# Kernel tuning notes

Hardware: AMD Instinct MI355X
Metric: run time of the kernel (lower is better)

## Reference

```python
import jax, jax.numpy as jnp
import numpy as np

B, S, D, H = 4, 4096, 1024, 16
DV = D // H


def setup_inputs() -> dict:
    key = jax.random.key(0)
    ks = jax.random.split(key, 8)
    def gl(k, shape):  # glorot-uniform-ish init
        fan_in, fan_out = shape[0], shape[-1]
        lim = np.sqrt(6.0 / (fan_in + fan_out)).astype(np.float32)
        return jax.random.uniform(k, shape, jnp.float32, -lim, lim)
    return {
        "q": jax.random.normal(ks[0], (B, S, D), jnp.float32),
        "k": jax.random.normal(ks[1], (B, S, D), jnp.float32),
        "v": jax.random.normal(ks[2], (B, S, D), jnp.float32),
        "wq": gl(ks[3], (D, H)), "bq": jnp.zeros((H,), jnp.float32),
        "wk": gl(ks[4], (D, H)), "bk": jnp.zeros((H,), jnp.float32),
        "wv": gl(ks[5], (D, D)), "bv": jnp.zeros((D,), jnp.float32),
        "wo": gl(ks[6], (D, D)), "bo": jnp.zeros((D,), jnp.float32),
    }


def reference(q, k, v, wq, bq, wk, bk, wv, bv, wo, bo):
    b, s, d = q.shape
    h = wq.shape[1]
    dv = d // h
    # per-head scalar queries/keys, sigmoid feature map phi
    qh = jax.nn.sigmoid(q @ wq + bq)                 # (B,S,H)
    kh = jax.nn.sigmoid(k @ wk + bk)                 # (B,S,H)
    vh = (v @ wv + bv).reshape(b, s, h, dv)          # (B,S,H,DV)
    # phi(k)^T @ v contracts seq -> per-head summary (B,H,DV)
    kv = jnp.einsum("bsh,bshd->bhd", kh, vh)
    # NOTE: original tf code cumsums over axis=1 of (B,H,1,DV): the HEAD axis
    state = jnp.cumsum(kv, axis=1)                   # (B,H,DV)
    # phi(q) @ state, broadcast over seq
    out_h = jnp.einsum("bsh,bhd->bshd", qh, state)   # (B,S,H,DV)
    concat = out_h.reshape(b, s, d)
    return concat @ wo + bo                          # (B,S,D)
```

## Files before the change

kernel.cpp:

```cpp
#include <hip/hip_runtime.h>

#define SS 4096
#define DD 1024
#define HH 16

typedef float nfloat4 __attribute__((ext_vector_type(4)));
typedef __attribute__((ext_vector_type(8))) short bf16x8;
typedef __attribute__((ext_vector_type(4))) float f32x4;

__device__ __forceinline__ short f2bf(float f) {
  union { float f; unsigned u; } z; z.f = f;
  return (short)((z.u + 0x8000u) >> 16);
}

__global__ __launch_bounds__(256) void k_wfrag(
    const float* __restrict__ wq, const float* __restrict__ wk,
    short* __restrict__ wf)
{
  const int m = blockIdx.x;
  const float* __restrict__ w = m ? wk : wq;
  short* __restrict__ dst = wf + m * 16384;
  for (int p = threadIdx.x; p < 2048; p += 256) {
    const int t = p >> 6, l = p & 63;
    const int kbase = t*32 + ((l >> 4) * 8), col = l & 15;
    short v[8];
#pragma unroll
    for (int e = 0; e < 8; ++e)
      v[e] = f2bf(w[(size_t)(kbase + e)*HH + col]);
    short* o = dst + (size_t)p * 8;
#pragma unroll
    for (int e = 0; e < 8; ++e) o[e] = v[e];
  }
}

__global__ __launch_bounds__(256, 4) void k_kh(
    const float* __restrict__ k, const short* __restrict__ wf,
    const float* __restrict__ bk, float* __restrict__ kh,
    float* __restrict__ ksp)
{
  const int t = threadIdx.x;
  const int wid = t >> 6, lane = t & 63;
  const int s0 = blockIdx.x * 16;
  const short* __restrict__ wfm = wf + 16384;

  __shared__ float smem[16 * 516];

  bf16x8 afrag[8];
#pragma unroll
  for (int i = 0; i < 8; ++i) {
    const int st = (i < 4) ? (wid*4 + i) : (16 + wid*4 + (i - 4));
    afrag[i] = *(const bf16x8*)(wfm + (size_t)(st*64 + lane) * 8);
  }

  const int row = lane & 15, g = lane >> 4;
  f32x4 acc = {0.f, 0.f, 0.f, 0.f};
#pragma unroll
  for (int hf = 0; hf < 2; ++hf) {
    const int r0 = wid * 4;
#pragma unroll
    for (int rr = 0; rr < 4; ++rr) {
      const int r = r0 + rr;
      const float* gsrc = k + (size_t)(s0 + r)*DD + hf*512 + lane*4;
      float* lbase = smem + r*516;
#pragma unroll
      for (int sg = 0; sg < 2; ++sg) {
        __builtin_amdgcn_global_load_lds(
            (const __attribute__((address_space(1))) void*)(gsrc + sg*256),
            (__attribute__((address_space(3))) void*)(lbase + sg*256),
            16, 0, 0);
      }
    }
    __syncthreads();
    const float* __restrict__ xrow = smem + row*516 + wid*128 + g*8;
#pragma unroll
    for (int tt = 0; tt < 4; ++tt) {
      const float4 lo = *(const float4*)(xrow + tt*32);
      const float4 hi = *(const float4*)(xrow + tt*32 + 4);
      bf16x8 bb;
      bb[0]=f2bf(lo.x); bb[1]=f2bf(lo.y); bb[2]=f2bf(lo.z); bb[3]=f2bf(lo.w);
      bb[4]=f2bf(hi.x); bb[5]=f2bf(hi.y); bb[6]=f2bf(hi.z); bb[7]=f2bf(hi.w);
      acc = __builtin_amdgcn_mfma_f32_16x16x32_bf16(afrag[hf*4+tt], bb, acc, 0, 0, 0);
    }
    __syncthreads();
  }
  float* red = smem;
  *(f32x4*)&red[(wid*64 + lane)*4] = acc;
  __syncthreads();
  const int orow = t >> 4, ohead = t & 15;
  const int lane2 = ((ohead >> 2) << 4) + orow;
  const int j = ohead & 3;
  const float sacc = red[0*256 + lane2*4 + j] + red[1*256 + lane2*4 + j]
                   + red[2*256 + lane2*4 + j] + red[3*256 + lane2*4 + j];
  const float sig = 1.f/(1.f + __expf(-(sacc + bk[ohead])));
  kh[(size_t)(s0 + orow)*HH + ohead] = sig;
  __syncthreads();
  smem[t] = sig;
  __syncthreads();
  if (t < 16) {
    float s = 0.f;
#pragma unroll
    for (int r = 0; r < 16; ++r) s += smem[r*16 + t];
    ksp[blockIdx.x*16 + t] = s;
  }
}

__global__ __launch_bounds__(256, 8) void k_kvt(
    const float* __restrict__ v, const float* __restrict__ kh,
    float* __restrict__ part)
{
  const int schunk = blockIdx.x;
  const int dchunk = blockIdx.y;
  const int b = blockIdx.z;
  const int t = threadIdx.x;
  const int c = t & 31;
  const int hh2 = (t >> 5) & 1;
  const int g = t >> 6;
  const int d0 = dchunk*128 + c*4;
  float acc[8][4];
#pragma unroll
  for (int h = 0; h < 8; ++h) {
    acc[h][0] = 0.f; acc[h][1] = 0.f; acc[h][2] = 0.f; acc[h][3] = 0.f;
  }
#pragma unroll 2
  for (int jj = 0; jj < 32; ++jj) {
    const int s = (jj*4 + g)*32 + schunk;
    const size_t rb = (size_t)(b*SS + s);
    const float4 v4 = *(const float4*)(v + rb*DD + d0);
    const float4* khp = (const float4*)(kh + rb*HH) + hh2*2;
    const float4 k0 = khp[0], k1 = khp[1];
    const float kk[8] = {k0.x,k0.y,k0.z,k0.w, k1.x,k1.y,k1.z,k1.w};
#pragma unroll
    for (int h = 0; h < 8; ++h) {
      acc[h][0] = fmaf(kk[h], v4.x, acc[h][0]);
      acc[h][1] = fmaf(kk[h], v4.y, acc[h][1]);
      acc[h][2] = fmaf(kk[h], v4.z, acc[h][2]);
      acc[h][3] = fmaf(kk[h], v4.w, acc[h][3]);
    }
  }
  __shared__ float lds[4][2][128];
  const size_t pbase = (size_t)((b*8 + dchunk)*32 + schunk) * 2048;
#pragma unroll
  for (int h = 0; h < 8; ++h) {
    *(float4*)&lds[g][hh2][c*4] =
        make_float4(acc[h][0], acc[h][1], acc[h][2], acc[h][3]);
    __syncthreads();
    {
      const int hh2r = t >> 7, dl = t & 127;
      const float sum = lds[0][hh2r][dl] + lds[1][hh2r][dl]
                      + lds[2][hh2r][dl] + lds[3][hh2r][dl];
      part[pbase + (hh2r*8 + h)*128 + dl] = sum;
    }
    __syncthreads();
  }
}

__global__ __launch_bounds__(256, 8) void k_red(
    const float* __restrict__ part, float* __restrict__ kvt)
{
  const int dchunk = blockIdx.x;
  const int b = blockIdx.y;
  const int hq = blockIdx.z;
  const int t = threadIdx.x;
  const size_t pb = (size_t)((b*8 + dchunk)*32) * 2048;
#pragma unroll
  for (int ho = 0; ho < 2; ++ho) {
    const int h = hq*4 + ho*2 + (t >> 7), dl = t & 127;
    float s = 0.f;
#pragma unroll 8
    for (int sc = 0; sc < 32; ++sc)
      s += part[pb + (size_t)sc*2048 + h*128 + dl];
    kvt[(size_t)(b*16 + h)*1024 + dchunk*128 + dl] = s;
  }
}

__global__ __launch_bounds__(256, 4) void k_kv(
    const float* __restrict__ kvt, const float* __restrict__ wv,
    float* __restrict__ kvp)
{
  const int h = blockIdx.x;
  const int b = blockIdx.y;
  const int dq = blockIdx.z;
  const int t = threadIdx.x;
  const int w = t >> 6, lane = t & 63;
  __shared__ float kvs[256];
  __shared__ float red[256];
  kvs[t] = kvt[(size_t)(b*16 + h)*1024 + dq*256 + t];
  __syncthreads();
  const float* __restrict__ wp = wv + (size_t)(dq*256 + w*64)*DD + h*64 + lane;
  float acc = 0.f;
#pragma unroll 16
  for (int i = 0; i < 64; ++i)
    acc = fmaf(kvs[w*64 + i], wp[(size_t)i*DD], acc);
  red[t] = acc;
  __syncthreads();
  if (t < 64)
    kvp[((size_t)(b*16 + h)*4 + dq)*64 + t] =
        red[t] + red[64+t] + red[128+t] + red[192+t];
}

__global__ __launch_bounds__(256) void k_kvfin(
    const float* __restrict__ kvp, const float* __restrict__ ksp,
    const float* __restrict__ bv, float* __restrict__ kv)
{
  const int b = blockIdx.x;
  const int t = threadIdx.x;
  __shared__ float red[256];
  __shared__ float ksum[16];
  float s = 0.f;
#pragma unroll
  for (int m = 0; m < 16; ++m)
    s += ksp[b*4096 + m*256 + t];
  red[t] = s;
  __syncthreads();
  if (t < 16) {
    float ks = 0.f;
#pragma unroll
    for (int g = 0; g < 16; ++g) ks += red[g*16 + t];
    ksum[t] = ks;
  }
  __syncthreads();
#pragma unroll
  for (int j = 0; j < 4; ++j) {
    const int idx = j*256 + t;
    const int h = idx >> 6;
    const float* kp = kvp + (size_t)(b*16 + h)*256 + (idx & 63);
    kv[(size_t)b*1024 + idx] =
        kp[0] + kp[64] + kp[128] + kp[192] + ksum[h]*bv[idx];
  }
}

__global__ __launch_bounds__(256) void k_w2(
    const float* __restrict__ kv, const float* __restrict__ wo,
    float* __restrict__ W2)
{
  const int bh = blockIdx.x;
  const int b = bh >> 4, h = bh & 15;
  const int t = threadIdx.x;
  __shared__ float st[64];
  if (t < 64) {
    float s = 0.f;
    for (int hp = 0; hp <= h; ++hp) s += kv[(size_t)b*1024 + hp*64 + t];
    st[t] = s;
  }
  __syncthreads();
  const int d0 = t * 4;
  float4 acc = {0.f, 0.f, 0.f, 0.f};
#pragma unroll 4
  for (int dv = 0; dv < 64; ++dv) {
    const float sv = st[dv];
    const float4 w4 = *(const float4*)(wo + (size_t)(h*64 + dv)*DD + d0);
    acc.x = fmaf(sv, w4.x, acc.x);
    acc.y = fmaf(sv, w4.y, acc.y);
    acc.z = fmaf(sv, w4.z, acc.z);
    acc.w = fmaf(sv, w4.w, acc.w);
  }
  *(float4*)(W2 + (size_t)(b*HH + h)*DD + d0) = acc;
}

__global__ __launch_bounds__(256, 4) void k_qout(
    const float* __restrict__ q, const short* __restrict__ wf,
    const float* __restrict__ bq, const float* __restrict__ W2,
    const float* __restrict__ bo, float* __restrict__ out)
{
  const int t = threadIdx.x;
  const int wid = t >> 6, lane = t & 63;
  const int tile = blockIdx.x;
  const int b = tile >> 8;
  const int s0 = tile * 16;

  __shared__ float smem[16 * 516];

  float4 w2[16];
  {
    const float* w2p = W2 + (size_t)(b*HH)*DD + t*4;
#pragma unroll
    for (int h = 0; h < 16; ++h) w2[h] = *(const float4*)(w2p + h*DD);
  }
  const float4 bo4 = *(const float4*)(bo + t*4);

  bf16x8 afrag[8];
#pragma unroll
  for (int i = 0; i < 8; ++i) {
    const int st = (i < 4) ? (wid*4 + i) : (16 + wid*4 + (i - 4));
    afrag[i] = *(const bf16x8*)(wf + (size_t)(st*64 + lane) * 8);
  }

  const int row = lane & 15, g = lane >> 4;
  f32x4 acc = {0.f, 0.f, 0.f, 0.f};
#pragma unroll
  for (int hf = 0; hf < 2; ++hf) {
    const int r0 = wid * 4;
#pragma unroll
    for (int rr = 0; rr < 4; ++rr) {
      const int r = r0 + rr;
      const float* gsrc = q + (size_t)(s0 + r)*DD + hf*512 + lane*4;
      float* lbase = smem + r*516;
#pragma unroll
      for (int sg = 0; sg < 2; ++sg) {
        __builtin_amdgcn_global_load_lds(
            (const __attribute__((address_space(1))) void*)(gsrc + sg*256),
            (__attribute__((address_space(3))) void*)(lbase + sg*256),
            16, 0, 0);
      }
    }
    __syncthreads();
    const float* __restrict__ xrow = smem + row*516 + wid*128 + g*8;
#pragma unroll
    for (int tt = 0; tt < 4; ++tt) {
      const float4 lo = *(const float4*)(xrow + tt*32);
      const float4 hi = *(const float4*)(xrow + tt*32 + 4);
      bf16x8 bb;
      bb[0]=f2bf(lo.x); bb[1]=f2bf(lo.y); bb[2]=f2bf(lo.z); bb[3]=f2bf(lo.w);
      bb[4]=f2bf(hi.x); bb[5]=f2bf(hi.y); bb[6]=f2bf(hi.z); bb[7]=f2bf(hi.w);
      acc = __builtin_amdgcn_mfma_f32_16x16x32_bf16(afrag[hf*4+tt], bb, acc, 0, 0, 0);
    }
    __syncthreads();
  }
  float* red = smem;
  *(f32x4*)&red[(wid*64 + lane)*4] = acc;
  __syncthreads();
  {
    const int orow = t >> 4, ohead = t & 15;
    const int lane2 = ((ohead >> 2) << 4) + orow;
    const int j = ohead & 3;
    const float sacc = red[0*256 + lane2*4 + j] + red[1*256 + lane2*4 + j]
                     + red[2*256 + lane2*4 + j] + red[3*256 + lane2*4 + j];
    const float val = sacc + bq[ohead];
    smem[1024 + orow*16 + ohead] = 1.f/(1.f + __expf(-val));
  }
  __syncthreads();

  const float* qs = smem + 1024;
#pragma unroll
  for (int r = 0; r < 16; ++r) {
    float4 o = bo4;
#pragma unroll
    for (int h = 0; h < 16; ++h) {
      const float qv = qs[r*16 + h];
      o.x = fmaf(qv, w2[h].x, o.x);
      o.y = fmaf(qv, w2[h].y, o.y);
      o.z = fmaf(qv, w2[h].z, o.z);
      o.w = fmaf(qv, w2[h].w, o.w);
    }
    nfloat4 ov = { o.x, o.y, o.z, o.w };
    nfloat4* dst = (nfloat4*)(out + (size_t)(s0 + r)*DD + t*4);
    __builtin_nontemporal_store(ov, dst);
  }
}

extern "C" void kernel_launch(void* const* d_in, const int* in_sizes, int n_in,
                              void* d_out, int out_size, void* d_ws, size_t ws_size,
                              hipStream_t stream)
{
  const float* q  = (const float*)d_in[0];
  const float* k  = (const float*)d_in[1];
  const float* v  = (const float*)d_in[2];
  const float* wq = (const float*)d_in[3];
  const float* bq = (const float*)d_in[4];
  const float* wk = (const float*)d_in[5];
  const float* bk = (const float*)d_in[6];
  const float* wv = (const float*)d_in[7];
  const float* bv = (const float*)d_in[8];
  const float* wo = (const float*)d_in[9];
  const float* bo = (const float*)d_in[10];
  float* out = (float*)d_out;
  float* ws  = (float*)d_ws;

  float* kh  = ws;
  float* kvt = ws + 262144;
  float* kvp = ws + 327680;
  float* ksp = ws + 344064;
  float* kv  = ws + 360448;
  float* W2  = ws + 364544;
  short* wf  = (short*)(ws + 430080);
  float* part = out;

  hipLaunchKernelGGL(k_wfrag, dim3(2), dim3(256), 0, stream,
                     wq, wk, wf);
  hipLaunchKernelGGL(k_kh, dim3(1024), dim3(256), 0, stream,
                     k, wf, bk, kh, ksp);
  hipLaunchKernelGGL(k_kvt, dim3(32, 8, 4), dim3(256), 0, stream,
                     v, kh, part);
  hipLaunchKernelGGL(k_red, dim3(8, 4, 4), dim3(256), 0, stream,
                     part, kvt);
  hipLaunchKernelGGL(k_kv, dim3(16, 4, 4), dim3(256), 0, stream,
                     kvt, wv, kvp);
  hipLaunchKernelGGL(k_kvfin, dim3(4), dim3(256), 0, stream,
                     kvp, ksp, bv, kv);
  hipLaunchKernelGGL(k_w2, dim3(64), dim3(256), 0, stream,
                     kv, wo, W2);
  hipLaunchKernelGGL(k_qout, dim3(1024), dim3(256), 0, stream,
                     q, wf, bq, W2, bo, out);
}
```

Baseline: 89.39 us.

## Double-buffer q/k row staging in LDS across four quarter-chunks

The k_kh and k_qout projection loops now split each row into four 256-float quarters, staged into two LDS buffers with async global_load_lds. Explicit vmcnt waits and barriers let the next quarter's loads overlap the current quarter's MFMA work. The weight-fragment indexing is remapped to match the new K split. In k_qout the W2 and bias register loads move after the MFMA loop, which shortens the period they hold registers. The hand-written vmcnt counts depend on how the compiler orders instructions, so a wrong count could read LDS before the data arrives.

```diff
diff --git a/kernel.cpp b/kernel.cpp
--- a/kernel.cpp
+++ b/kernel.cpp
@@ -3,6 +3,7 @@
 #define SS 4096
 #define DD 1024
 #define HH 16
+#define PITCH 260
 
 typedef float nfloat4 __attribute__((ext_vector_type(4)));
 typedef __attribute__((ext_vector_type(8))) short bf16x8;
@@ -43,46 +44,56 @@
   const int s0 = blockIdx.x * 16;
   const short* __restrict__ wfm = wf + 16384;
 
-  __shared__ float smem[16 * 516];
+  __shared__ float smem[2*16*PITCH + 256];
+  float* const buf0 = smem;
+  float* const buf1 = smem + 16*PITCH;
 
   bf16x8 afrag[8];
 #pragma unroll
   for (int i = 0; i < 8; ++i) {
-    const int st = (i < 4) ? (wid*4 + i) : (16 + wid*4 + (i - 4));
+    const int st = (i >> 1)*8 + wid*2 + (i & 1);
     afrag[i] = *(const bf16x8*)(wfm + (size_t)(st*64 + lane) * 8);
   }
+
+#define STAGE_K(bp, qd)                                                      \
+  {                                                                          \
+    const int r0_ = wid*4;                                                   \
+    _Pragma("unroll")                                                        \
+    for (int rr_ = 0; rr_ < 4; ++rr_) {                                      \
+      const int r_ = r0_ + rr_;                                              \
+      __builtin_amdgcn_global_load_lds(                                      \
+          (const __attribute__((address_space(1))) void*)                    \
+              (k + (size_t)(s0 + r_)*DD + (qd)*256 + lane*4),                \
+          (__attribute__((address_space(3))) void*)((bp) + r_*PITCH + lane*4), \
+          16, 0, 0);                                                         \
+    }                                                                        \
+  }
+
+  STAGE_K(buf0, 0);
+  STAGE_K(buf1, 1);
 
   const int row = lane & 15, g = lane >> 4;
   f32x4 acc = {0.f, 0.f, 0.f, 0.f};
 #pragma unroll
-  for (int hf = 0; hf < 2; ++hf) {
-    const int r0 = wid * 4;
-#pragma unroll
-    for (int rr = 0; rr < 4; ++rr) {
-      const int r = r0 + rr;
-      const float* gsrc = k + (size_t)(s0 + r)*DD + hf*512 + lane*4;
-      float* lbase = smem + r*516;
-#pragma unroll
-      for (int sg = 0; sg < 2; ++sg) {
-        __builtin_amdgcn_global_load_lds(
-            (const __attribute__((address_space(1))) void*)(gsrc + sg*256),
-            (__attribute__((address_space(3))) void*)(lbase + sg*256),
-            16, 0, 0);
-      }
-    }
-    __syncthreads();
-    const float* __restrict__ xrow = smem + row*516 + wid*128 + g*8;
-#pragma unroll
-    for (int tt = 0; tt < 4; ++tt) {
+  for (int qd = 0; qd < 4; ++qd) {
+    if (qd < 3) asm volatile("s_waitcnt vmcnt(4)" ::: "memory");
+    else        asm volatile("s_waitcnt vmcnt(0)" ::: "memory");
+    __builtin_amdgcn_s_barrier();
+    const float* bp = (qd & 1) ? buf1 : buf0;
+    const float* xrow = bp + row*PITCH + wid*64 + g*8;
+#pragma unroll
+    for (int tt = 0; tt < 2; ++tt) {
       const float4 lo = *(const float4*)(xrow + tt*32);
       const float4 hi = *(const float4*)(xrow + tt*32 + 4);
       bf16x8 bb;
       bb[0]=f2bf(lo.x); bb[1]=f2bf(lo.y); bb[2]=f2bf(lo.z); bb[3]=f2bf(lo.w);
       bb[4]=f2bf(hi.x); bb[5]=f2bf(hi.y); bb[6]=f2bf(hi.z); bb[7]=f2bf(hi.w);
-      acc = __builtin_amdgcn_mfma_f32_16x16x32_bf16(afrag[hf*4+tt], bb, acc, 0, 0, 0);
+      acc = __builtin_amdgcn_mfma_f32_16x16x32_bf16(afrag[qd*2+tt], bb, acc, 0, 0, 0);
     }
-    __syncthreads();
-  }
+    __builtin_amdgcn_s_barrier();
+    if (qd < 2) STAGE_K(((qd & 1) ? buf1 : buf0), qd + 2);
+  }
+
   float* red = smem;
   *(f32x4*)&red[(wid*64 + lane)*4] = acc;
   __syncthreads();
@@ -94,12 +105,13 @@
   const float sig = 1.f/(1.f + __expf(-(sacc + bk[ohead])));
   kh[(size_t)(s0 + orow)*HH + ohead] = sig;
   __syncthreads();
-  smem[t] = sig;
+  float* sg = smem + 2*16*PITCH;
+  sg[t] = sig;
   __syncthreads();
   if (t < 16) {
     float s = 0.f;
 #pragma unroll
-    for (int r = 0; r < 16; ++r) s += smem[r*16 + t];
+    for (int r = 0; r < 16; ++r) s += sg[r*16 + t];
     ksp[blockIdx.x*16 + t] = s;
   }
 }
@@ -268,54 +280,64 @@
   const int b = tile >> 8;
   const int s0 = tile * 16;
 
-  __shared__ float smem[16 * 516];
-
-  float4 w2[16];
-  {
-    const float* w2p = W2 + (size_t)(b*HH)*DD + t*4;
-#pragma unroll
-    for (int h = 0; h < 16; ++h) w2[h] = *(const float4*)(w2p + h*DD);
-  }
-  const float4 bo4 = *(const float4*)(bo + t*4);
+  __shared__ float smem[2*16*PITCH + 256];
+  float* const buf0 = smem;
+  float* const buf1 = smem + 16*PITCH;
 
   bf16x8 afrag[8];
 #pragma unroll
   for (int i = 0; i < 8; ++i) {
-    const int st = (i < 4) ? (wid*4 + i) : (16 + wid*4 + (i - 4));
+    const int st = (i >> 1)*8 + wid*2 + (i & 1);
     afrag[i] = *(const bf16x8*)(wf + (size_t)(st*64 + lane) * 8);
   }
+
+#define STAGE_Q(bp, qd)                                                      \
+  {                                                                          \
+    const int r0_ = wid*4;                                                   \
+    _Pragma("unroll")                                                        \
+    for (int rr_ = 0; rr_ < 4; ++rr_) {                                      \
+      const int r_ = r0_ + rr_;                                              \
+      __builtin_amdgcn_global_load_lds(                                      \
+          (const __attribute__((address_space(1))) void*)                    \
+              (q + (size_t)(s0 + r_)*DD + (qd)*256 + lane*4),                \
+          (__attribute__((address_space(3))) void*)((bp) + r_*PITCH + lane*4), \
+          16, 0, 0);                                                         \
+    }                                                                        \
+  }
+
+  STAGE_Q(buf0, 0);
+  STAGE_Q(buf1, 1);
 
   const int row = lane & 15, g = lane >> 4;
   f32x4 acc = {0.f, 0.f, 0.f, 0.f};
 #pragma unroll
-  for (int hf = 0; hf < 2; ++hf) {
-    const int r0 = wid * 4;
-#pragma unroll
-    for (int rr = 0; rr < 4; ++rr) {
-      const int r = r0 + rr;
-      const float* gsrc = q + (size_t)(s0 + r)*DD + hf*512 + lane*4;
-      float* lbase = smem + r*516;
-#pragma unroll
-      for (int sg = 0; sg < 2; ++sg) {
-        __builtin_amdgcn_global_load_lds(
-            (const __attribute__((address_space(1))) void*)(gsrc + sg*256),
-            (__attribute__((address_space(3))) void*)(lbase + sg*256),
-            16, 0, 0);
-      }
-    }
-    __syncthreads();
-    const float* __restrict__ xrow = smem + row*516 + wid*128 + g*8;
-#pragma unroll
-    for (int tt = 0; tt < 4; ++tt) {
+  for (int qd = 0; qd < 4; ++qd) {
+    if (qd < 3) asm volatile("s_waitcnt vmcnt(4)" ::: "memory");
+    else        asm volatile("s_waitcnt vmcnt(0)" ::: "memory");
+    __builtin_amdgcn_s_barrier();
+    const float* bp = (qd & 1) ? buf1 : buf0;
+    const float* xrow = bp + row*PITCH + wid*64 + g*8;
+#pragma unroll
+    for (int tt = 0; tt < 2; ++tt) {
       const float4 lo = *(const float4*)(xrow + tt*32);
       const float4 hi = *(const float4*)(xrow + tt*32 + 4);
       bf16x8 bb;
       bb[0]=f2bf(lo.x); bb[1]=f2bf(lo.y); bb[2]=f2bf(lo.z); bb[3]=f2bf(lo.w);
       bb[4]=f2bf(hi.x); bb[5]=f2bf(hi.y); bb[6]=f2bf(hi.z); bb[7]=f2bf(hi.w);
-      acc = __builtin_amdgcn_mfma_f32_16x16x32_bf16(afrag[hf*4+tt], bb, acc, 0, 0, 0);
+      acc = __builtin_amdgcn_mfma_f32_16x16x32_bf16(afrag[qd*2+tt], bb, acc, 0, 0, 0);
     }
-    __syncthreads();
-  }
+    __builtin_amdgcn_s_barrier();
+    if (qd < 2) STAGE_Q(((qd & 1) ? buf1 : buf0), qd + 2);
+  }
+
+  float4 w2[16];
+  {
+    const float* w2p = W2 + (size_t)(b*HH)*DD + t*4;
+#pragma unroll
+    for (int h = 0; h < 16; ++h) w2[h] = *(const float4*)(w2p + h*DD);
+  }
+  const float4 bo4 = *(const float4*)(bo + t*4);
+
   float* red = smem;
   *(f32x4*)&red[(wid*64 + lane)*4] = acc;
   __syncthreads();
@@ -326,11 +348,11 @@
     const float sacc = red[0*256 + lane2*4 + j] + red[1*256 + lane2*4 + j]
                      + red[2*256 + lane2*4 + j] + red[3*256 + lane2*4 + j];
     const float val = sacc + bq[ohead];
-    smem[1024 + orow*16 + ohead] = 1.f/(1.f + __expf(-val));
-  }
-  __syncthreads();
-
-  const float* qs = smem + 1024;
+    smem[2*16*PITCH + orow*16 + ohead] = 1.f/(1.f + __expf(-val));
+  }
+  __syncthreads();
+
+  const float* qs = smem + 2*16*PITCH;
 #pragma unroll
   for (int r = 0; r < 16; ++r) {
     float4 o = bo4;
```

New measurement: 88.99 us. No clear change (-0.5%).
